# Kernel optimization log

Hardware: AMD Instinct MI355X
Metric: run time of the kernel (lower is better)

Reference implementation:

```python
import jax, jax.numpy as jnp
import numpy as np

B, S, D, H = 2, 2048, 1024, 16
HD = D // H  # head_dim = 64

def setup_inputs() -> dict:
    key = jax.random.key(0)
    ks = jax.random.split(key, 11)
    s = 1.0 / np.sqrt(D)
    return {
        "query_input": jax.random.normal(ks[0], (B, S, D), jnp.float32),
        "key_input":   jax.random.normal(ks[1], (B, S, D), jnp.float32),
        "value_input": jax.random.normal(ks[2], (B, S, D), jnp.float32),
        "Wq": jax.random.normal(ks[3], (D, D), jnp.float32) * s,
        "bq": jnp.zeros((D,), jnp.float32),
        "Wk": jax.random.normal(ks[4], (D, D), jnp.float32) * s,
        "bk": jnp.zeros((D,), jnp.float32),
        "Wv": jax.random.normal(ks[5], (D, D), jnp.float32) * s,
        "bv": jnp.zeros((D,), jnp.float32),
        "Wo": jax.random.normal(ks[6], (D, D), jnp.float32) * s,
        "bo": jnp.zeros((D,), jnp.float32),
    }

def _split_heads(x):
    b, s, _ = x.shape
    return x.reshape(b, s, H, HD).transpose(0, 2, 1, 3)  # [B,H,S,HD]

def reference(query_input, key_input, value_input, Wq, bq, Wk, bk, Wv, bv, Wo, bo):
    q = _split_heads(query_input @ Wq + bq)
    k = _split_heads(key_input @ Wk + bk)
    v = _split_heads(value_input @ Wv + bv)
    scores = jnp.einsum('bhqd,bhkd->bhqk', q, k) / jnp.sqrt(jnp.float32(HD))
    attn = jax.nn.softmax(scores, axis=-1)
    out = jnp.einsum('bhqk,bhkd->bhqd', attn, v)
    out = out.transpose(0, 2, 1, 3).reshape(query_input.shape[0], -1, H * HD)
    return out @ Wo + bo
```

## Files before the change

kernel.cpp:

```cpp
#include <hip/hip_runtime.h>
#include <hip/hip_bf16.h>
#include <math.h>

#define B_  2
#define S_  2048
#define D_  1024
#define H_  16
#define HD_ 64

typedef __bf16  bf16x8  __attribute__((ext_vector_type(8)));
typedef float   floatx4 __attribute__((ext_vector_type(4)));

#define MFMA16(a, b, c) __builtin_amdgcn_mfma_f32_16x16x32_bf16((a), (b), (c), 0, 0, 0)

__device__ __forceinline__ void load_lds16(const void* g, void* l) {
    __builtin_amdgcn_global_load_lds(
        (const __attribute__((address_space(1))) unsigned int*)g,
        (__attribute__((address_space(3))) unsigned int*)l, 16, 0, 0);
}

__global__ __launch_bounds__(256) void cast3_bf16_k(
    const float* __restrict__ x0, const float* __restrict__ x1, const float* __restrict__ x2,
    __hip_bfloat16* __restrict__ o0, __hip_bfloat16* __restrict__ o1, __hip_bfloat16* __restrict__ o2)
{
    const int z = blockIdx.y;
    const float* src = (z == 0) ? x0 : (z == 1) ? x1 : x2;
    __hip_bfloat16* dst = (z == 0) ? o0 : (z == 1) ? o1 : o2;
    const int i = blockIdx.x * 256 + threadIdx.x;
    const float4* s4 = (const float4*)src;
    const float4 a = s4[2 * i + 0];
    const float4 b = s4[2 * i + 1];
    union { __hip_bfloat16 h[8]; uint4 v; } p;
    p.h[0] = __float2bfloat16(a.x); p.h[1] = __float2bfloat16(a.y);
    p.h[2] = __float2bfloat16(a.z); p.h[3] = __float2bfloat16(a.w);
    p.h[4] = __float2bfloat16(b.x); p.h[5] = __float2bfloat16(b.y);
    p.h[6] = __float2bfloat16(b.z); p.h[7] = __float2bfloat16(b.w);
    ((uint4*)dst)[i] = p.v;
}

__global__ __launch_bounds__(256) void transpose4_cast_k(
    const float* __restrict__ W0, const float* __restrict__ W1,
    const float* __restrict__ W2, const float* __restrict__ W3,
    __hip_bfloat16* __restrict__ T0, __hip_bfloat16* __restrict__ T1,
    __hip_bfloat16* __restrict__ T2, __hip_bfloat16* __restrict__ T3)
{
    const int z = blockIdx.z;
    const float* W = (z == 0) ? W0 : (z == 1) ? W1 : (z == 2) ? W2 : W3;
    __hip_bfloat16* Wt = (z == 0) ? T0 : (z == 1) ? T1 : (z == 2) ? T2 : T3;

    __shared__ float T[64][65];
    const int t  = threadIdx.x;
    const int n0 = blockIdx.x * 64, k0 = blockIdx.y * 64;
    #pragma unroll
    for (int i = 0; i < 4; ++i) {
        const int u = t + i * 256;
        const int r = u >> 4, c4 = (u & 15) * 4;
        const float4 v = *(const float4*)(W + (size_t)(k0 + r) * D_ + n0 + c4);
        T[r][c4 + 0] = v.x; T[r][c4 + 1] = v.y; T[r][c4 + 2] = v.z; T[r][c4 + 3] = v.w;
    }
    __syncthreads();
    #pragma unroll
    for (int i = 0; i < 4; ++i) {
        const int u = t + i * 256;
        const int n = u >> 4, c4 = (u & 15) * 4;
        union { __hip_bfloat16 h[4]; uint2 v; } p;
        #pragma unroll
        for (int j = 0; j < 4; ++j) p.h[j] = __float2bfloat16(T[c4 + j][n]);
        *(uint2*)(Wt + (size_t)(n0 + n) * D_ + k0 + c4) = p.v;
    }
}

__global__ __launch_bounds__(256) void gemm_qkv_k(
    const __hip_bfloat16* __restrict__ xq, const __hip_bfloat16* __restrict__ xk,
    const __hip_bfloat16* __restrict__ xv,
    const __hip_bfloat16* __restrict__ WqT, const __hip_bfloat16* __restrict__ WkT,
    const __hip_bfloat16* __restrict__ WvT,
    const float* __restrict__ bq, const float* __restrict__ bk, const float* __restrict__ bv,
    __hip_bfloat16* __restrict__ Qh, __hip_bfloat16* __restrict__ Kh,
    __hip_bfloat16* __restrict__ Vt)
{
    constexpr int K = 1024;
    __shared__ __align__(16) short As0[4][128][8], As1[4][128][8];
    __shared__ __align__(16) short Bs0[4][128][8], Bs1[4][128][8];

    const int z = blockIdx.z;
    const __hip_bfloat16* A  = (z == 0) ? xq  : (z == 1) ? xk  : xv;
    const __hip_bfloat16* Bt = (z == 0) ? WqT : (z == 1) ? WkT : WvT;
    const float* bias        = (z == 0) ? bq  : (z == 1) ? bk  : bv;

    const int t    = threadIdx.x;
    const int lane = t & 63, w = t >> 6;
    const int quad = lane >> 4, l16 = lane & 15;
    const int m0   = blockIdx.x * 128, n0 = blockIdx.y * 128;
    const int wm   = (w >> 1) * 64,    wn = (w & 1) * 64;

    floatx4 acc[4][4] = {};

    auto stage = [&](int k0, short (*As)[128][8], short (*Bs)[128][8]) {
        #pragma unroll
        for (int i = 0; i < 2; ++i) {
            const int c = t + i * 256;
            const int kq = c >> 7, m = c & 127;
            load_lds16(A + (size_t)(m0 + m) * K + k0 + kq * 8, &As[kq][m][0]);
        }
        #pragma unroll
        for (int i = 0; i < 2; ++i) {
            const int c = t + i * 256;
            const int kq = c >> 7, n = c & 127;
            load_lds16(Bt + (size_t)(n0 + n) * K + k0 + kq * 8, &Bs[kq][n][0]);
        }
    };

    auto compute = [&](short (*As)[128][8], short (*Bs)[128][8]) {
        bf16x8 af[4], bfr[4];
        #pragma unroll
        for (int mt = 0; mt < 4; ++mt) af[mt]  = *(const bf16x8*)&As[quad][wm + mt * 16 + l16][0];
        #pragma unroll
        for (int nt = 0; nt < 4; ++nt) bfr[nt] = *(const bf16x8*)&Bs[quad][wn + nt * 16 + l16][0];
        #pragma unroll
        for (int mt = 0; mt < 4; ++mt)
            #pragma unroll
            for (int nt = 0; nt < 4; ++nt)
                acc[mt][nt] = MFMA16(af[mt], bfr[nt], acc[mt][nt]);
    };

    stage(0, As0, Bs0);
    for (int k0 = 0; k0 < K; k0 += 64) {
        __syncthreads();
        stage(k0 + 32, As1, Bs1);
        compute(As0, Bs0);
        __syncthreads();
        if (k0 + 64 < K) stage(k0 + 64, As0, Bs0);
        compute(As1, Bs1);
    }

    const float oscale = (z == 0) ? 0.125f : 1.0f;
    __hip_bfloat16* outp = (z == 0) ? Qh : (z == 1) ? Kh : Vt;

    #pragma unroll
    for (int mt = 0; mt < 4; ++mt)
        #pragma unroll
        for (int nt = 0; nt < 4; ++nt) {
            const int gn = n0 + wn + nt * 16 + l16;
            const float bi = bias[gn];
            #pragma unroll
            for (int r = 0; r < 4; ++r) {
                const int gm = m0 + wm + mt * 16 + quad * 4 + r;
                const float v = (acc[mt][nt][r] + bi) * oscale;
                if (z != 2) {
                    outp[(((size_t)(gm >> 11) * H_ + (gn >> 6)) * S_ + (gm & 2047)) * 64 + (gn & 63)] =
                        __float2bfloat16(v);
                } else {
                    outp[(((size_t)(gm >> 11) * H_ + (gn >> 6)) * 64 + (gn & 63)) * S_ + (gm & 2047)] =
                        __float2bfloat16(v);
                }
            }
        }
}

__global__ __launch_bounds__(256) void gemm_oproj_k(
    const __hip_bfloat16* __restrict__ A, const __hip_bfloat16* __restrict__ Bt,
    const float* __restrict__ bias, float* __restrict__ out)
{
    constexpr int K = 1024, N = 1024;
    __shared__ __align__(16) short As0[4][128][8], As1[4][128][8];
    __shared__ __align__(16) short Bs0[4][64][8],  Bs1[4][64][8];

    const int t    = threadIdx.x;
    const int lane = t & 63, w = t >> 6;
    const int quad = lane >> 4, l16 = lane & 15;
    const int m0   = blockIdx.x * 128, n0 = blockIdx.y * 64;
    const int wm   = (w >> 1) * 64,    wn = (w & 1) * 32;

    floatx4 acc[4][2] = {};

    auto stage = [&](int k0, short (*As)[128][8], short (*Bs)[64][8]) {
        #pragma unroll
        for (int i = 0; i < 2; ++i) {
            const int c = t + i * 256;
            const int kq = c >> 7, m = c & 127;
            load_lds16(A + (size_t)(m0 + m) * K + k0 + kq * 8, &As[kq][m][0]);
        }
        {
            const int kq = t >> 6, n = t & 63;
            load_lds16(Bt + (size_t)(n0 + n) * K + k0 + kq * 8, &Bs[kq][n][0]);
        }
    };

    auto compute = [&](short (*As)[128][8], short (*Bs)[64][8]) {
        bf16x8 af[4], bfr[2];
        #pragma unroll
        for (int mt = 0; mt < 4; ++mt) af[mt]  = *(const bf16x8*)&As[quad][wm + mt * 16 + l16][0];
        #pragma unroll
        for (int nt = 0; nt < 2; ++nt) bfr[nt] = *(const bf16x8*)&Bs[quad][wn + nt * 16 + l16][0];
        #pragma unroll
        for (int mt = 0; mt < 4; ++mt)
            #pragma unroll
            for (int nt = 0; nt < 2; ++nt)
                acc[mt][nt] = MFMA16(af[mt], bfr[nt], acc[mt][nt]);
    };

    stage(0, As0, Bs0);
    for (int k0 = 0; k0 < K; k0 += 64) {
        __syncthreads();
        stage(k0 + 32, As1, Bs1);
        compute(As0, Bs0);
        __syncthreads();
        if (k0 + 64 < K) stage(k0 + 64, As0, Bs0);
        compute(As1, Bs1);
    }

    #pragma unroll
    for (int mt = 0; mt < 4; ++mt)
        #pragma unroll
        for (int nt = 0; nt < 2; ++nt) {
            const int gn = n0 + wn + nt * 16 + l16;
            const float bi = bias[gn];
            #pragma unroll
            for (int r = 0; r < 4; ++r) {
                const int gm = m0 + wm + mt * 16 + quad * 4 + r;
                out[(size_t)gm * N + gn] = acc[mt][nt][r] + bi;
            }
        }
}

__global__ __launch_bounds__(512) void attn_mfma_k(
    const __hip_bfloat16* __restrict__ Qh, const __hip_bfloat16* __restrict__ Kh,
    const __hip_bfloat16* __restrict__ Vt, __hip_bfloat16* __restrict__ Ctx)
{
    __shared__ __align__(16) short Ks0[8][64][8], Ks1[8][64][8];
    __shared__ __align__(16) short Vs0[8][64][8], Vs1[8][64][8];
    __shared__ __align__(16) __hip_bfloat16 Ps[128][72];

    const int t    = threadIdx.x;
    const int lane = t & 63, w = t >> 6;
    const int quad = lane >> 4, l16 = lane & 15;
    const int b = blockIdx.z, h = blockIdx.x;
    const size_t bh = (size_t)b * H_ + h;
    const int q0 = blockIdx.y * 128;
    const int myrow = w * 16;

    bf16x8 qf[2];
    {
        const __hip_bfloat16* qb = Qh + (bh * S_ + q0 + myrow + l16) * 64;
        qf[0] = *(const bf16x8*)(qb + quad * 8);
        qf[1] = *(const bf16x8*)(qb + 32 + quad * 8);
    }

    floatx4 oacc[4] = {};
    float lsum[4] = {0.f, 0.f, 0.f, 0.f};

    auto stage = [&](int kt, short (*Ks)[64][8], short (*Vs)[64][8]) {
        const int kq = t >> 6, p = t & 63;
        load_lds16(Kh + (bh * S_ + kt * 64 + p) * 64 + kq * 8, &Ks[kq][p][0]);
        load_lds16(Vt + (bh * 64 + p) * S_ + kt * 64 + kq * 8, &Vs[kq][p][0]);
    };

    auto compute = [&](short (*Ks)[64][8], short (*Vs)[64][8]) {
        floatx4 sacc[4] = {};
        #pragma unroll
        for (int ks = 0; ks < 2; ++ks)
            #pragma unroll
            for (int nt = 0; nt < 4; ++nt) {
                const bf16x8 kf = *(const bf16x8*)&Ks[ks * 4 + quad][nt * 16 + l16][0];
                sacc[nt] = MFMA16(qf[ks], kf, sacc[nt]);
            }
        #pragma unroll
        for (int nt = 0; nt < 4; ++nt)
            #pragma unroll
            for (int r = 0; r < 4; ++r) {
                const float p = __expf(sacc[nt][r]);
                lsum[r] += p;
                Ps[myrow + quad * 4 + r][nt * 16 + l16] = __float2bfloat16(p);
            }
        #pragma unroll
        for (int ks = 0; ks < 2; ++ks) {
            const bf16x8 pf = *(const bf16x8*)&Ps[myrow + l16][ks * 32 + quad * 8];
            #pragma unroll
            for (int nt = 0; nt < 4; ++nt) {
                const bf16x8 vf = *(const bf16x8*)&Vs[ks * 4 + quad][nt * 16 + l16][0];
                oacc[nt] = MFMA16(pf, vf, oacc[nt]);
            }
        }
    };

    stage(0, Ks0, Vs0);
    for (int kt = 0; kt < S_ / 64; kt += 2) {
        __syncthreads();
        stage(kt + 1, Ks1, Vs1);
        compute(Ks0, Vs0);
        __syncthreads();
        if (kt + 2 < S_ / 64) stage(kt + 2, Ks0, Vs0);
        compute(Ks1, Vs1);
    }

    #pragma unroll
    for (int off = 1; off < 16; off <<= 1)
        #pragma unroll
        for (int r = 0; r < 4; ++r) lsum[r] += __shfl_xor(lsum[r], off, 64);

    #pragma unroll
    for (int nt = 0; nt < 4; ++nt)
        #pragma unroll
        for (int r = 0; r < 4; ++r) {
            const int qrow = q0 + myrow + quad * 4 + r;
            Ctx[((size_t)b * S_ + qrow) * D_ + h * 64 + nt * 16 + l16] =
                __float2bfloat16(oacc[nt][r] / lsum[r]);
        }
}

extern "C" void kernel_launch(void* const* d_in, const int* in_sizes, int n_in,
                              void* d_out, int out_size, void* d_ws, size_t ws_size,
                              hipStream_t stream)
{
    const float* xq = (const float*)d_in[0];
    const float* xk = (const float*)d_in[1];
    const float* xv = (const float*)d_in[2];
    const float* Wq = (const float*)d_in[3];
    const float* bq = (const float*)d_in[4];
    const float* Wk = (const float*)d_in[5];
    const float* bk = (const float*)d_in[6];
    const float* Wv = (const float*)d_in[7];
    const float* bv = (const float*)d_in[8];
    const float* Wo = (const float*)d_in[9];
    const float* bo = (const float*)d_in[10];
    float* out = (float*)d_out;

    const size_t n = (size_t)B_ * S_ * D_;
    char* p = (char*)d_ws;
    __hip_bfloat16* xqb = (__hip_bfloat16*)p;            p += n * 2;
    __hip_bfloat16* xkb = (__hip_bfloat16*)p;            p += n * 2;
    __hip_bfloat16* xvb = (__hip_bfloat16*)p;            p += n * 2;
    __hip_bfloat16* WqT = (__hip_bfloat16*)p;            p += (size_t)D_ * D_ * 2;
    __hip_bfloat16* WkT = (__hip_bfloat16*)p;            p += (size_t)D_ * D_ * 2;
    __hip_bfloat16* WvT = (__hip_bfloat16*)p;            p += (size_t)D_ * D_ * 2;
    __hip_bfloat16* WoT = (__hip_bfloat16*)p;            p += (size_t)D_ * D_ * 2;
    __hip_bfloat16* Qh  = (__hip_bfloat16*)p;            p += n * 2;
    __hip_bfloat16* Kh  = (__hip_bfloat16*)p;            p += n * 2;
    __hip_bfloat16* Vth = (__hip_bfloat16*)p;            p += n * 2;
    __hip_bfloat16* Ctx = (__hip_bfloat16*)p;            p += n * 2;

    cast3_bf16_k<<<dim3((int)(n / 8 / 256), 3), dim3(256), 0, stream>>>(
        xq, xk, xv, xqb, xkb, xvb);
    transpose4_cast_k<<<dim3(16, 16, 4), dim3(256), 0, stream>>>(
        Wq, Wk, Wv, Wo, WqT, WkT, WvT, WoT);

    gemm_qkv_k<<<dim3((B_ * S_) / 128, D_ / 128, 3), dim3(256), 0, stream>>>(
        xqb, xkb, xvb, WqT, WkT, WvT, bq, bk, bv, Qh, Kh, Vth);

    attn_mfma_k<<<dim3(H_, S_ / 128, B_), dim3(512), 0, stream>>>(Qh, Kh, Vth, Ctx);

    gemm_oproj_k<<<dim3((B_ * S_) / 128, D_ / 64), dim3(256), 0, stream>>>(
        Ctx, WoT, bo, out);
}
```

Measured before the change: 254.3 us.

## Use row-major XOR-swizzled LDS tiles and packed V-transpose stores

Changes the LDS staging layout in the QKV GEMM, the output-projection GEMM and the attention kernel from k-chunk-major to row-major with an XOR swizzle on the 16-byte chunk index. Each global-to-LDS load now reads contiguous 64-byte or 128-byte row segments instead of strided 16-byte pieces, and the fragment reads apply the swizzle to avoid bank conflicts. The V-projection epilogue also packs four bf16 values into one 8-byte store instead of four scalar stores to the transposed layout. The cost is extra index arithmetic in both staging and fragment reads.

```diff
diff --git a/kernel.cpp b/kernel.cpp
--- a/kernel.cpp
+++ b/kernel.cpp
@@ -80,8 +80,8 @@
     __hip_bfloat16* __restrict__ Vt)
 {
     constexpr int K = 1024;
-    __shared__ __align__(16) short As0[4][128][8], As1[4][128][8];
-    __shared__ __align__(16) short Bs0[4][128][8], Bs1[4][128][8];
+    __shared__ __align__(16) short As0[128][32], As1[128][32];
+    __shared__ __align__(16) short Bs0[128][32], Bs1[128][32];
 
     const int z = blockIdx.z;
     const __hip_bfloat16* A  = (z == 0) ? xq  : (z == 1) ? xk  : xv;
@@ -96,27 +96,33 @@
 
     floatx4 acc[4][4] = {};
 
-    auto stage = [&](int k0, short (*As)[128][8], short (*Bs)[128][8]) {
+    auto stage = [&](int k0, short (*As)[32], short (*Bs)[32]) {
         #pragma unroll
         for (int i = 0; i < 2; ++i) {
             const int c = t + i * 256;
-            const int kq = c >> 7, m = c & 127;
-            load_lds16(A + (size_t)(m0 + m) * K + k0 + kq * 8, &As[kq][m][0]);
+            const int m = c >> 2, kq = (c ^ (m >> 1)) & 3;
+            load_lds16(A + (size_t)(m0 + m) * K + k0 + kq * 8, &As[0][0] + c * 8);
         }
         #pragma unroll
         for (int i = 0; i < 2; ++i) {
             const int c = t + i * 256;
-            const int kq = c >> 7, n = c & 127;
-            load_lds16(Bt + (size_t)(n0 + n) * K + k0 + kq * 8, &Bs[kq][n][0]);
-        }
-    };
-
-    auto compute = [&](short (*As)[128][8], short (*Bs)[128][8]) {
+            const int n = c >> 2, kq = (c ^ (n >> 1)) & 3;
+            load_lds16(Bt + (size_t)(n0 + n) * K + k0 + kq * 8, &Bs[0][0] + c * 8);
+        }
+    };
+
+    auto compute = [&](short (*As)[32], short (*Bs)[32]) {
         bf16x8 af[4], bfr[4];
         #pragma unroll
-        for (int mt = 0; mt < 4; ++mt) af[mt]  = *(const bf16x8*)&As[quad][wm + mt * 16 + l16][0];
-        #pragma unroll
-        for (int nt = 0; nt < 4; ++nt) bfr[nt] = *(const bf16x8*)&Bs[quad][wn + nt * 16 + l16][0];
+        for (int mt = 0; mt < 4; ++mt) {
+            const int r = wm + mt * 16 + l16;
+            af[mt]  = *(const bf16x8*)&As[r][((quad ^ (r >> 1)) & 3) * 8];
+        }
+        #pragma unroll
+        for (int nt = 0; nt < 4; ++nt) {
+            const int n = wn + nt * 16 + l16;
+            bfr[nt] = *(const bf16x8*)&Bs[n][((quad ^ (n >> 1)) & 3) * 8];
+        }
         #pragma unroll
         for (int mt = 0; mt < 4; ++mt)
             #pragma unroll
@@ -134,28 +140,38 @@
         compute(As1, Bs1);
     }
 
-    const float oscale = (z == 0) ? 0.125f : 1.0f;
-    __hip_bfloat16* outp = (z == 0) ? Qh : (z == 1) ? Kh : Vt;
-
-    #pragma unroll
-    for (int mt = 0; mt < 4; ++mt)
-        #pragma unroll
-        for (int nt = 0; nt < 4; ++nt) {
-            const int gn = n0 + wn + nt * 16 + l16;
-            const float bi = bias[gn];
-            #pragma unroll
-            for (int r = 0; r < 4; ++r) {
-                const int gm = m0 + wm + mt * 16 + quad * 4 + r;
-                const float v = (acc[mt][nt][r] + bi) * oscale;
-                if (z != 2) {
+    if (z != 2) {
+        const float oscale = (z == 0) ? 0.125f : 1.0f;
+        __hip_bfloat16* outp = (z == 0) ? Qh : Kh;
+        #pragma unroll
+        for (int mt = 0; mt < 4; ++mt)
+            #pragma unroll
+            for (int nt = 0; nt < 4; ++nt) {
+                const int gn = n0 + wn + nt * 16 + l16;
+                const float bi = bias[gn];
+                #pragma unroll
+                for (int r = 0; r < 4; ++r) {
+                    const int gm = m0 + wm + mt * 16 + quad * 4 + r;
+                    const float v = (acc[mt][nt][r] + bi) * oscale;
                     outp[(((size_t)(gm >> 11) * H_ + (gn >> 6)) * S_ + (gm & 2047)) * 64 + (gn & 63)] =
                         __float2bfloat16(v);
-                } else {
-                    outp[(((size_t)(gm >> 11) * H_ + (gn >> 6)) * 64 + (gn & 63)) * S_ + (gm & 2047)] =
-                        __float2bfloat16(v);
                 }
             }
-        }
+    } else {
+        #pragma unroll
+        for (int mt = 0; mt < 4; ++mt)
+            #pragma unroll
+            for (int nt = 0; nt < 4; ++nt) {
+                const int gn = n0 + wn + nt * 16 + l16;
+                const float bi = bias[gn];
+                const int gm0 = m0 + wm + mt * 16 + quad * 4;
+                union { __hip_bfloat16 h[4]; uint2 u; } pk;
+                #pragma unroll
+                for (int r = 0; r < 4; ++r) pk.h[r] = __float2bfloat16(acc[mt][nt][r] + bi);
+                *(uint2*)(Vt + (((size_t)(gm0 >> 11) * H_ + (gn >> 6)) * 64 + (gn & 63)) * S_ +
+                          (gm0 & 2047)) = pk.u;
+            }
+    }
 }
 
 __global__ __launch_bounds__(256) void gemm_oproj_k(
@@ -163,8 +179,8 @@
     const float* __restrict__ bias, float* __restrict__ out)
 {
     constexpr int K = 1024, N = 1024;
-    __shared__ __align__(16) short As0[4][128][8], As1[4][128][8];
-    __shared__ __align__(16) short Bs0[4][64][8],  Bs1[4][64][8];
+    __shared__ __align__(16) short As0[128][32], As1[128][32];
+    __shared__ __align__(16) short Bs0[64][32],  Bs1[64][32];
 
     const int t    = threadIdx.x;
     const int lane = t & 63, w = t >> 6;
@@ -174,25 +190,32 @@
 
     floatx4 acc[4][2] = {};
 
-    auto stage = [&](int k0, short (*As)[128][8], short (*Bs)[64][8]) {
+    auto stage = [&](int k0, short (*As)[32], short (*Bs)[32]) {
         #pragma unroll
         for (int i = 0; i < 2; ++i) {
             const int c = t + i * 256;
-            const int kq = c >> 7, m = c & 127;
-            load_lds16(A + (size_t)(m0 + m) * K + k0 + kq * 8, &As[kq][m][0]);
+            const int m = c >> 2, kq = (c ^ (m >> 1)) & 3;
+            load_lds16(A + (size_t)(m0 + m) * K + k0 + kq * 8, &As[0][0] + c * 8);
         }
         {
-            const int kq = t >> 6, n = t & 63;
-            load_lds16(Bt + (size_t)(n0 + n) * K + k0 + kq * 8, &Bs[kq][n][0]);
-        }
-    };
-
-    auto compute = [&](short (*As)[128][8], short (*Bs)[64][8]) {
+            const int c = t;
+            const int n = c >> 2, kq = (c ^ (n >> 1)) & 3;
+            load_lds16(Bt + (size_t)(n0 + n) * K + k0 + kq * 8, &Bs[0][0] + c * 8);
+        }
+    };
+
+    auto compute = [&](short (*As)[32], short (*Bs)[32]) {
         bf16x8 af[4], bfr[2];
         #pragma unroll
-        for (int mt = 0; mt < 4; ++mt) af[mt]  = *(const bf16x8*)&As[quad][wm + mt * 16 + l16][0];
-        #pragma unroll
-        for (int nt = 0; nt < 2; ++nt) bfr[nt] = *(const bf16x8*)&Bs[quad][wn + nt * 16 + l16][0];
+        for (int mt = 0; mt < 4; ++mt) {
+            const int r = wm + mt * 16 + l16;
+            af[mt]  = *(const bf16x8*)&As[r][((quad ^ (r >> 1)) & 3) * 8];
+        }
+        #pragma unroll
+        for (int nt = 0; nt < 2; ++nt) {
+            const int n = wn + nt * 16 + l16;
+            bfr[nt] = *(const bf16x8*)&Bs[n][((quad ^ (n >> 1)) & 3) * 8];
+        }
         #pragma unroll
         for (int mt = 0; mt < 4; ++mt)
             #pragma unroll
@@ -228,8 +251,8 @@
     const __hip_bfloat16* __restrict__ Qh, const __hip_bfloat16* __restrict__ Kh,
     const __hip_bfloat16* __restrict__ Vt, __hip_bfloat16* __restrict__ Ctx)
 {
-    __shared__ __align__(16) short Ks0[8][64][8], Ks1[8][64][8];
-    __shared__ __align__(16) short Vs0[8][64][8], Vs1[8][64][8];
+    __shared__ __align__(16) short Ks0[64][64], Ks1[64][64];
+    __shared__ __align__(16) short Vs0[64][64], Vs1[64][64];
     __shared__ __align__(16) __hip_bfloat16 Ps[128][72];
 
     const int t    = threadIdx.x;
@@ -250,35 +273,39 @@
     floatx4 oacc[4] = {};
     float lsum[4] = {0.f, 0.f, 0.f, 0.f};
 
-    auto stage = [&](int kt, short (*Ks)[64][8], short (*Vs)[64][8]) {
-        const int kq = t >> 6, p = t & 63;
-        load_lds16(Kh + (bh * S_ + kt * 64 + p) * 64 + kq * 8, &Ks[kq][p][0]);
-        load_lds16(Vt + (bh * 64 + p) * S_ + kt * 64 + kq * 8, &Vs[kq][p][0]);
-    };
-
-    auto compute = [&](short (*Ks)[64][8], short (*Vs)[64][8]) {
+    auto stage = [&](int kt, short (*Ks)[64], short (*Vs)[64]) {
+        const int p = t >> 3, kq = (t ^ p) & 7;
+        load_lds16(Kh + (bh * S_ + kt * 64 + p) * 64 + kq * 8, &Ks[0][0] + t * 8);
+        load_lds16(Vt + (bh * 64 + p) * S_ + kt * 64 + kq * 8, &Vs[0][0] + t * 8);
+    };
+
+    auto compute = [&](short (*Ks)[64], short (*Vs)[64]) {
         floatx4 sacc[4] = {};
         #pragma unroll
         for (int ks = 0; ks < 2; ++ks)
             #pragma unroll
             for (int nt = 0; nt < 4; ++nt) {
-                const bf16x8 kf = *(const bf16x8*)&Ks[ks * 4 + quad][nt * 16 + l16][0];
+                const int p  = nt * 16 + l16;
+                const int ch = ks * 4 + quad;
+                const bf16x8 kf = *(const bf16x8*)&Ks[p][((ch ^ p) & 7) * 8];
                 sacc[nt] = MFMA16(qf[ks], kf, sacc[nt]);
             }
         #pragma unroll
         for (int nt = 0; nt < 4; ++nt)
             #pragma unroll
             for (int r = 0; r < 4; ++r) {
-                const float p = __expf(sacc[nt][r]);
-                lsum[r] += p;
-                Ps[myrow + quad * 4 + r][nt * 16 + l16] = __float2bfloat16(p);
+                const float pv = __expf(sacc[nt][r]);
+                lsum[r] += pv;
+                Ps[myrow + quad * 4 + r][nt * 16 + l16] = __float2bfloat16(pv);
             }
         #pragma unroll
         for (int ks = 0; ks < 2; ++ks) {
             const bf16x8 pf = *(const bf16x8*)&Ps[myrow + l16][ks * 32 + quad * 8];
             #pragma unroll
             for (int nt = 0; nt < 4; ++nt) {
-                const bf16x8 vf = *(const bf16x8*)&Vs[ks * 4 + quad][nt * 16 + l16][0];
+                const int hd = nt * 16 + l16;
+                const int ch = ks * 4 + quad;
+                const bf16x8 vf = *(const bf16x8*)&Vs[hd][((ch ^ hd) & 7) * 8];
                 oacc[nt] = MFMA16(pf, vf, oacc[nt]);
             }
         }
```

After: 228.8 us. 1.11x faster.
